# Performance work log

Hardware: AMD Instinct MI355X
Metric: run time of the kernel (lower is better)

## Reference

```python
import jax, jax.numpy as jnp
import numpy as np

DIM = 768
NUM_HEADS = 12
HEAD_DIM = DIM // NUM_HEADS
SCALE = HEAD_DIM ** -0.5
B, N = 16, 640  # N = 8*8 + 24*24


def setup_inputs() -> dict:
    key = jax.random.key(0)
    ks = jax.random.split(key, 4)
    x = jax.random.normal(ks[0], (B, N, DIM), dtype=jnp.float32)
    # weights stored input-major: y = x @ W + b (equiv. to torch Linear with W = weight.T)
    qkv_w = jax.random.normal(ks[1], (DIM, 3 * DIM), dtype=jnp.float32) * (DIM ** -0.5)
    qkv_b = jnp.zeros((3 * DIM,), dtype=jnp.float32)
    proj_w = jax.random.normal(ks[2], (DIM, DIM), dtype=jnp.float32) * (DIM ** -0.5)
    proj_b = jnp.zeros((DIM,), dtype=jnp.float32)
    w = jnp.ones((2,), dtype=jnp.float32)
    return {"x": x, "qkv_w": qkv_w, "qkv_b": qkv_b, "proj_w": proj_w,
            "proj_b": proj_b, "w": w, "t_h": 8, "t_w": 8, "s_h": 24, "s_w": 24}


def reference(x, qkv_w, qkv_b, proj_w, proj_b, w, t_h, t_w, s_h, s_w):
    b, n, c = x.shape
    qkv = (x @ qkv_w + qkv_b).reshape(b, n, 3, NUM_HEADS, HEAD_DIM)
    qkv = jnp.transpose(qkv, (2, 0, 3, 1, 4))  # [3, B, H, N, D]
    q, k, v = qkv[0], qkv[1], qkv[2]
    attn = jnp.einsum('bhnd,bhmd->bhnm', q, k) * SCALE  # [B,H,N,N]
    attn0 = jax.nn.softmax(attn, axis=-1)
    attn1 = jnp.square(jax.nn.relu(attn))
    ws = jax.nn.softmax(w)  # exp(w_i)/sum(exp(w)) blend weights
    attn = attn0 * ws[0] + attn1 * ws[1]
    out = jnp.einsum('bhnm,bhmd->bhnd', attn, v)  # [B,H,N,D]
    out = jnp.transpose(out, (0, 2, 1, 3)).reshape(b, n, c)
    return out @ proj_w + proj_b
```

## Files before the change

### kernel.cpp

```cpp
#include <hip/hip_runtime.h>
#include <hip/hip_bf16.h>

typedef __attribute__((ext_vector_type(8))) short short8;
typedef __attribute__((ext_vector_type(4))) float floatx4;
typedef __hip_bfloat16 bf16;

#define DIM 768
#define NH 12
#define HD 64
#define BB 16
#define NN 640
#define BH (BB*NH)
#define MROWS (BB*NN)
#define QKVN (3*DIM)
#define QSCALE 0.18033688011113205f
#define LN2SQ 0.4804530139182014f

#define CVT_BLK (MROWS*DIM/4/256)
#define TRQ_BLK ((QKVN/32)*(DIM/32))
#define TRP_BLK ((DIM/32)*(DIM/32))

__device__ __forceinline__ floatx4 mfma16(short8 a, short8 b, floatx4 c) {
    return __builtin_amdgcn_mfma_f32_16x16x32_bf16(a, b, c, 0, 0, 0);
}

__device__ __forceinline__ void async_ld16(const bf16* g, bf16* l) {
    __builtin_amdgcn_global_load_lds(
        (const __attribute__((address_space(1))) void*)g,
        (__attribute__((address_space(3))) void*)l, 16, 0, 0);
}

__device__ __forceinline__ unsigned pack_trunc(float a, float b) {
    return __builtin_amdgcn_perm(__float_as_uint(b), __float_as_uint(a), 0x07060302u);
}

__device__ __forceinline__ unsigned pack_rne(float a, float b) {
    unsigned sa = (unsigned)__bfloat16_as_ushort(__float2bfloat16(a));
    unsigned sb = (unsigned)__bfloat16_as_ushort(__float2bfloat16(b));
    return sa | (sb << 16);
}

__device__ __forceinline__ float fexp2(float x) {
#if __has_builtin(__builtin_amdgcn_exp2f)
    return __builtin_amdgcn_exp2f(x);
#else
    return exp2f(x);
#endif
}

__global__ void prep_all(const float* __restrict__ x,
                         const float* __restrict__ qkv_w,
                         const float* __restrict__ proj_w,
                         bf16* __restrict__ xb,
                         bf16* __restrict__ qwT,
                         bf16* __restrict__ pwT)
{
    __shared__ float tile[32][33];
    const int id = blockIdx.x;
    const int t = threadIdx.x;

    if (id < CVT_BLK) {
        int i = id * 256 + t;
        float4 v = ((const float4*)x)[i];
        *(uint2*)(xb + (size_t)i * 4) =
            make_uint2(pack_rne(v.x, v.y), pack_rne(v.z, v.w));
        return;
    }

    const float* src; bf16* dst; int C, bx, by;
    if (id < CVT_BLK + TRQ_BLK) {
        int j = id - CVT_BLK;
        bx = j % (QKVN/32); by = j / (QKVN/32);
        src = qkv_w; dst = qwT; C = QKVN;
    } else {
        int j = id - CVT_BLK - TRQ_BLK;
        bx = j % (DIM/32); by = j / (DIM/32);
        src = proj_w; dst = pwT; C = DIM;
    }
    const int R = DIM;
    const int tx = t & 31, ty = t >> 5;
    for (int j = 0; j < 4; ++j)
        tile[ty + j*8][tx] = src[(size_t)(by*32 + ty + j*8) * C + bx*32 + tx];
    __syncthreads();
    for (int j = 0; j < 4; ++j)
        dst[(size_t)(bx*32 + ty + j*8) * R + by*32 + tx] = __float2bfloat16(tile[tx][ty + j*8]);
}

template<int MODE>
__global__ __launch_bounds__(256) void gemm_bt(
    const bf16* __restrict__ A, const bf16* __restrict__ B, const float* __restrict__ bias,
    int M, int N, int K,
    bf16* __restrict__ outb, bf16* __restrict__ vTo, float* __restrict__ outf)
{
    __shared__ __align__(16) bf16 As[2][128*64];
    __shared__ __align__(16) bf16 Bs[2][128*64];

    const int t = threadIdx.x;
    const int lane = t & 63, wave = t >> 6;
    const int l15 = lane & 15, quad = lane >> 4;
    const int wm = (wave >> 1) * 64, wn = (wave & 1) * 64;

    constexpr int GX  = (MODE == 0) ? (QKVN/128) : (DIM/128);
    constexpr int NWG = GX * (MROWS/128);
    constexpr int CHUNK = NWG / 8;
    int lin = blockIdx.y * GX + blockIdx.x;
    lin = (lin & 7) * CHUNK + (lin >> 3);
    const int m0 = (lin / GX) * 128, n0 = (lin % GX) * 128;

    floatx4 acc[4][4];
    floatx4 zero = {0.f, 0.f, 0.f, 0.f};
    for (int i = 0; i < 4; ++i)
        for (int j = 0; j < 4; ++j)
            acc[i][j] = zero;

    const int trow = t >> 3;
    const int gc = ((t & 7) ^ (trow & 7)) << 3;
    const bf16* aA = A + (size_t)(m0 + trow) * K + gc;
    const bf16* aB = B + (size_t)(n0 + trow) * K + gc;
    const int lb = wave * 512;

    for (int s = 0; s < 4; ++s) {
        async_ld16(aA + (size_t)s*32*K, &As[0][s*2048 + lb]);
        async_ld16(aB + (size_t)s*32*K, &Bs[0][s*2048 + lb]);
    }

    const int sw = l15 & 7;
    const int nit = K >> 6;
    for (int kt = 0; kt < nit; ++kt) {
        const int cur = kt & 1;
        __syncthreads();
        if (kt + 1 < nit) {
            const bf16* pA = aA + (size_t)(kt+1)*64;
            const bf16* pB = aB + (size_t)(kt+1)*64;
            for (int s = 0; s < 4; ++s) {
                async_ld16(pA + (size_t)s*32*K, &As[cur^1][s*2048 + lb]);
                async_ld16(pB + (size_t)s*32*K, &Bs[cur^1][s*2048 + lb]);
            }
        }
        short8 af0[4], af1[4], bf0[4], bf1[4];
        for (int fm = 0; fm < 4; ++fm) {
            int base = (wm + fm*16 + l15) * 64 + ((quad ^ sw) << 3);
            af0[fm] = *(const short8*)(&As[cur][base]);
            af1[fm] = *(const short8*)(&As[cur][base ^ 32]);
        }
        for (int fn = 0; fn < 4; ++fn) {
            int base = (wn + fn*16 + l15) * 64 + ((quad ^ sw) << 3);
            bf0[fn] = *(const short8*)(&Bs[cur][base]);
            bf1[fn] = *(const short8*)(&Bs[cur][base ^ 32]);
        }
        for (int fm = 0; fm < 4; ++fm)
            for (int fn = 0; fn < 4; ++fn) {
                acc[fm][fn] = mfma16(bf0[fn], af0[fm], acc[fm][fn]);
                acc[fm][fn] = mfma16(bf1[fn], af1[fm], acc[fm][fn]);
            }
    }

    if (MODE == 0 && n0 >= 2*DIM) {
        bf16* S = &As[0][0] + wave * 2048;
        unsigned short* Su = (unsigned short*)S;
        const int bh   = (m0 / NN) * NH + ((n0 + wn) >> 6) - 24;
        const int tokb = (m0 % NN) + wm;
        const int dl = lane >> 2, cc = (lane & 3) * 16;
        for (int fn = 0; fn < 4; ++fn) {
            int nb = n0 + wn + fn*16 + quad*4;
            float4 bv = *(const float4*)(bias + nb);
            float bvr[4] = {bv.x, bv.y, bv.z, bv.w};
            for (int fm = 0; fm < 4; ++fm) {
#pragma unroll
                for (int r = 0; r < 4; ++r) {
                    float v = acc[fm][fn][r] + bvr[r];
                    Su[(quad*4 + r)*72 + fm*16 + l15] =
                        (unsigned short)(__float_as_uint(v) >> 16);
                }
            }
            uint4 r0 = *(const uint4*)(S + dl*72 + cc);
            uint4 r1 = *(const uint4*)(S + dl*72 + cc + 8);
            bf16* dst = vTo + ((size_t)bh * HD + fn*16 + dl) * NN + tokb + cc;
            *(uint4*)dst = r0;
            *(uint4*)(dst + 8) = r1;
        }
        return;
    }

    for (int fm = 0; fm < 4; ++fm) {
        int m = m0 + wm + fm*16 + l15;
        if (MODE == 0) {
            bf16* row = outb + (size_t)m * N;
            for (int fn = 0; fn < 4; ++fn) {
                int n = n0 + wn + fn*16 + quad*4;
                float4 bv = *(const float4*)(bias + n);
                float v0 = acc[fm][fn][0] + bv.x;
                float v1 = acc[fm][fn][1] + bv.y;
                float v2 = acc[fm][fn][2] + bv.z;
                float v3 = acc[fm][fn][3] + bv.w;
                if (n < DIM) {
                    v0 *= QSCALE; v1 *= QSCALE; v2 *= QSCALE; v3 *= QSCALE;
                }
                *(uint2*)(row + n) = make_uint2(pack_rne(v0, v1), pack_rne(v2, v3));
            }
        } else {
            float* row = outf + (size_t)m * N;
            for (int fn = 0; fn < 4; ++fn) {
                int n = n0 + wn + fn*16 + quad*4;
                float4 bv = *(const float4*)(bias + n);
                float4 v;
                v.x = acc[fm][fn][0] + bv.x;
                v.y = acc[fm][fn][1] + bv.y;
                v.z = acc[fm][fn][2] + bv.z;
                v.w = acc[fm][fn][3] + bv.w;
                *(float4*)(row + n) = v;
            }
        }
    }
}

__global__ __launch_bounds__(256) void attn_kernel(
    const bf16* __restrict__ qkv, const bf16* __restrict__ vT,
    const float* __restrict__ w2, bf16* __restrict__ ao)
{
    int lin = blockIdx.y * BH + blockIdx.x;
    int j = lin >> 3;
    const int bh = (lin & 7) + 8 * (j / 10);
    const int qt = j % 10;
    const int b = bh / NH, h = bh - b * NH;
    const int t = threadIdx.x;
    const int wave = t >> 6, lane = t & 63;
    const int l15 = lane & 15, quad = lane >> 4;
    const int qrow0 = qt * 64 + wave * 16;

    float w0 = w2[0], w1 = w2[1];
    float wmx = fmaxf(w0, w1);
    float e0 = __expf(w0 - wmx), e1 = __expf(w1 - wmx);
    float ws0 = e0 / (e0 + e1);
    float ws1 = (1.0f - ws0) * LN2SQ;

    __shared__ __align__(16) bf16 Kb[2][64*64];
    __shared__ __align__(16) bf16 Vb[2][64*64];
    __shared__ __align__(16) bf16 Ps[4][16*72];
    __shared__ __align__(16) bf16 Pr[4][16*72];

    const bf16* kb = qkv + (size_t)(b*NN)*QKVN + DIM + h*HD;
    const bf16* vb = vT + (size_t)bh * HD * NN;

    const bf16* qr = qkv + (size_t)(b*NN + qrow0 + l15) * QKVN + h*HD;
    short8 aq0 = *(const short8*)(qr + quad*8);
    short8 aq1 = *(const short8*)(qr + 32 + quad*8);

    const int srow = t >> 3;
    const int gc   = ((lane & 7) ^ (lane >> 3)) << 3;
    const bf16* kst = kb + (size_t)srow * QKVN + gc;
    const bf16* vst = vb + (size_t)srow * NN + gc;
    const int lb0 = (wave * 64) * 8;
    const int lb1 = (256 + wave * 64) * 8;

    async_ld16(kst,                     &Kb[0][lb0]);
    async_ld16(kst + (size_t)32 * QKVN, &Kb[0][lb1]);
    async_ld16(vst,                     &Vb[0][lb0]);
    async_ld16(vst + (size_t)32 * NN,   &Vb[0][lb1]);

    floatx4 zero = {0.f, 0.f, 0.f, 0.f};
    floatx4 accS[4], accR[4];
    for (int i = 0; i < 4; ++i) { accS[i] = zero; accR[i] = zero; }
    float lsum = 0.f;

    const int sw = l15 & 7;
    const int fbase = l15 * 64 + ((quad ^ sw) << 3);

    unsigned* PsW = (unsigned*)&Ps[wave][0];
    unsigned* PrW = (unsigned*)&Pr[wave][0];
    const int wb = l15*36 + quad*2;
    const bf16* PsR = &Ps[wave][l15*72 + quad*8];
    const bf16* PrR = &Pr[wave][l15*72 + quad*8];

#pragma unroll 2
    for (int kt = 0; kt < 10; ++kt) {
        const int cur = kt & 1;
        __syncthreads();
        if (kt + 1 < 10) {
            kst += (size_t)64 * QKVN;
            vst += 64;
            async_ld16(kst,                     &Kb[cur^1][lb0]);
            async_ld16(kst + (size_t)32 * QKVN, &Kb[cur^1][lb1]);
            async_ld16(vst,                     &Vb[cur^1][lb0]);
            async_ld16(vst + (size_t)32 * NN,   &Vb[cur^1][lb1]);
        }

        const bf16* Kc = &Kb[cur][0];
        const bf16* Vc = &Vb[cur][0];

        floatx4 s[4];
        for (int I = 0; I < 4; ++I) {
            short8 aklo = *(const short8*)(Kc + fbase + I*1024);
            short8 akhi = *(const short8*)(Kc + ((fbase + I*1024) ^ 32));
            s[I] = zero;
            s[I] = mfma16(aklo, aq0, s[I]);
            s[I] = mfma16(akhi, aq1, s[I]);
        }

        short8 bvlo[4], bvhi[4];
        for (int dt = 0; dt < 4; ++dt) {
            bvlo[dt] = *(const short8*)(Vc + fbase + dt*1024);
            bvhi[dt] = *(const short8*)(Vc + ((fbase + dt*1024) ^ 32));
        }

        for (int I = 0; I < 4; ++I) {
            float ex[4], rq[4];
            for (int r = 0; r < 4; ++r) {
                ex[r] = fexp2(s[I][r]);
                float m = fmaxf(s[I][r], 0.f);
                rq[r] = m * m;
                lsum += ex[r];
            }
            *(uint2*)(PsW + wb + I*8) = make_uint2(pack_trunc(ex[0],ex[1]), pack_trunc(ex[2],ex[3]));
            *(uint2*)(PrW + wb + I*8) = make_uint2(pack_trunc(rq[0],rq[1]), pack_trunc(rq[2],rq[3]));
        }

        short8 paSlo = *(const short8*)PsR;
        short8 paShi = *(const short8*)(PsR + 32);
        short8 paRlo = *(const short8*)PrR;
        short8 paRhi = *(const short8*)(PrR + 32);

        for (int dt = 0; dt < 4; ++dt) {
            accS[dt] = mfma16(paSlo, bvlo[dt], accS[dt]);
            accS[dt] = mfma16(paShi, bvhi[dt], accS[dt]);
            accR[dt] = mfma16(paRlo, bvlo[dt], accR[dt]);
            accR[dt] = mfma16(paRhi, bvhi[dt], accR[dt]);
        }
    }

    lsum += __shfl_xor(lsum, 16);
    lsum += __shfl_xor(lsum, 32);
    float invq[4];
    for (int r = 0; r < 4; ++r)
        invq[r] = 1.0f / __shfl(lsum, quad*4 + r);

    for (int dt = 0; dt < 4; ++dt) {
        for (int r = 0; r < 4; ++r) {
            float v = ws0 * accS[dt][r] * invq[r] + ws1 * accR[dt][r];
            int tok = qrow0 + quad*4 + r;
            ao[((size_t)(b * NN + tok)) * DIM + h * HD + dt*16 + l15] = __float2bfloat16(v);
        }
    }
}


extern "C" void kernel_launch(void* const* d_in, const int* in_sizes, int n_in,
                              void* d_out, int out_size, void* d_ws, size_t ws_size,
                              hipStream_t stream) {
    const float* x      = (const float*)d_in[0];
    const float* qkv_w  = (const float*)d_in[1];
    const float* qkv_b  = (const float*)d_in[2];
    const float* proj_w = (const float*)d_in[3];
    const float* proj_b = (const float*)d_in[4];
    const float* w2     = (const float*)d_in[5];
    float* out = (float*)d_out;

    bf16* xb   = (bf16*)d_ws;
    bf16* qwT  = xb   + (size_t)MROWS * DIM;
    bf16* pwT  = qwT  + (size_t)QKVN * DIM;
    bf16* qkvb = pwT  + (size_t)DIM * DIM;
    bf16* vT   = qkvb + (size_t)MROWS * QKVN;
    bf16* ao   = xb;

    prep_all<<<CVT_BLK + TRQ_BLK + TRP_BLK, 256, 0, stream>>>(
        x, qkv_w, proj_w, xb, qwT, pwT);

    gemm_bt<0><<<dim3(QKVN / 128, MROWS / 128), 256, 0, stream>>>(
        xb, qwT, qkv_b, MROWS, QKVN, DIM, qkvb, vT, nullptr);

    attn_kernel<<<dim3(BH, NN / 64), 256, 0, stream>>>(qkvb, vT, w2, ao);

    gemm_bt<1><<<dim3(DIM / 128, MROWS / 128), 256, 0, stream>>>(
        ao, pwT, proj_b, MROWS, DIM, DIM, nullptr, nullptr, out);
}
```

Before: 217.7 us.

## Use 128x192 tiles for QKV GEMM and 128-query attention blocks

Adds a dedicated QKV GEMM kernel with 128x192 output tiles (4x6 MFMA fragments per wave) and an XCD-aware block remap, splitting the V-transpose epilogue per 16-column fragment. The attention kernel now uses 512 threads covering 128 query rows per block, so each K/V tile loaded into LDS is shared by twice as many query rows, halving K/V global traffic. The larger accumulator arrays raise register pressure and the bigger attention blocks cut the block count, which may lower occupancy.

```diff
diff --git a/kernel.cpp b/kernel.cpp
--- a/kernel.cpp
+++ b/kernel.cpp
@@ -84,6 +84,139 @@
     __syncthreads();
     for (int j = 0; j < 4; ++j)
         dst[(size_t)(bx*32 + ty + j*8) * R + by*32 + tx] = __float2bfloat16(tile[tx][ty + j*8]);
+}
+
+__global__ __launch_bounds__(256) void gemm_qkv(
+    const bf16* __restrict__ A, const bf16* __restrict__ B, const float* __restrict__ bias,
+    bf16* __restrict__ outb, bf16* __restrict__ vTo)
+{
+    constexpr int K = DIM;
+    constexpr int N = QKVN;
+    constexpr int GX = N / 192;
+    constexpr int NWG = GX * (MROWS / 128);
+    constexpr int CHUNK = NWG / 8;
+
+    __shared__ __align__(16) bf16 As[2][128*64];
+    __shared__ __align__(16) bf16 Bs[2][192*64];
+
+    const int t = threadIdx.x;
+    const int lane = t & 63, wave = t >> 6;
+    const int l15 = lane & 15, quad = lane >> 4;
+    const int wm = (wave >> 1) * 64;
+    const int wn = (wave & 1) * 96;
+
+    int lin = blockIdx.x;
+    lin = (lin & 7) * CHUNK + (lin >> 3);
+    const int m0 = (lin / GX) * 128, n0 = (lin % GX) * 192;
+
+    floatx4 acc[4][6];
+    floatx4 zero = {0.f, 0.f, 0.f, 0.f};
+#pragma unroll
+    for (int i = 0; i < 4; ++i)
+#pragma unroll
+        for (int j = 0; j < 6; ++j)
+            acc[i][j] = zero;
+
+    const int trow = t >> 3;
+    const int gc = ((t & 7) ^ (trow & 7)) << 3;
+    const bf16* aA = A + (size_t)(m0 + trow) * K + gc;
+    const bf16* aB = B + (size_t)(n0 + trow) * K + gc;
+    const int lb = wave * 512;
+
+#pragma unroll
+    for (int s = 0; s < 4; ++s)
+        async_ld16(aA + (size_t)s*32*K, &As[0][s*2048 + lb]);
+#pragma unroll
+    for (int s = 0; s < 6; ++s)
+        async_ld16(aB + (size_t)s*32*K, &Bs[0][s*2048 + lb]);
+
+    const int sw = l15 & 7;
+    const int nit = K >> 6;
+    for (int kt = 0; kt < nit; ++kt) {
+        const int cur = kt & 1;
+        __syncthreads();
+        if (kt + 1 < nit) {
+            const bf16* pA = aA + (size_t)(kt+1)*64;
+            const bf16* pB = aB + (size_t)(kt+1)*64;
+#pragma unroll
+            for (int s = 0; s < 4; ++s)
+                async_ld16(pA + (size_t)s*32*K, &As[cur^1][s*2048 + lb]);
+#pragma unroll
+            for (int s = 0; s < 6; ++s)
+                async_ld16(pB + (size_t)s*32*K, &Bs[cur^1][s*2048 + lb]);
+        }
+        short8 af0[4], af1[4], bf0[6], bf1[6];
+#pragma unroll
+        for (int fm = 0; fm < 4; ++fm) {
+            int base = (wm + fm*16 + l15) * 64 + ((quad ^ sw) << 3);
+            af0[fm] = *(const short8*)(&As[cur][base]);
+            af1[fm] = *(const short8*)(&As[cur][base ^ 32]);
+        }
+#pragma unroll
+        for (int fn = 0; fn < 6; ++fn) {
+            int base = (wn + fn*16 + l15) * 64 + ((quad ^ sw) << 3);
+            bf0[fn] = *(const short8*)(&Bs[cur][base]);
+            bf1[fn] = *(const short8*)(&Bs[cur][base ^ 32]);
+        }
+#pragma unroll
+        for (int fm = 0; fm < 4; ++fm)
+#pragma unroll
+            for (int fn = 0; fn < 6; ++fn) {
+                acc[fm][fn] = mfma16(bf0[fn], af0[fm], acc[fm][fn]);
+                acc[fm][fn] = mfma16(bf1[fn], af1[fm], acc[fm][fn]);
+            }
+    }
+
+    const int mb = m0 + wm;
+    const int nb = n0 + wn;
+
+    if (n0 >= 2*DIM) {
+        bf16* S = &As[0][0] + wave * 2048;
+        unsigned short* Su = (unsigned short*)S;
+        const int batch = mb / NN;
+        const int tokb = mb % NN;
+        const int dl = lane >> 2, cc = (lane & 3) * 16;
+#pragma unroll
+        for (int fn = 0; fn < 6; ++fn) {
+            int cb = nb + fn*16;
+            int bh = batch * NH + ((cb - 2*DIM) >> 6);
+            int dbase = cb & 63;
+            float4 bv = *(const float4*)(bias + cb + quad*4);
+            float bvr[4] = {bv.x, bv.y, bv.z, bv.w};
+#pragma unroll
+            for (int fm = 0; fm < 4; ++fm) {
+#pragma unroll
+                for (int r = 0; r < 4; ++r) {
+                    float v = acc[fm][fn][r] + bvr[r];
+                    Su[(quad*4 + r)*72 + fm*16 + l15] =
+                        (unsigned short)(__float_as_uint(v) >> 16);
+                }
+            }
+            uint4 r0 = *(const uint4*)(S + dl*72 + cc);
+            uint4 r1 = *(const uint4*)(S + dl*72 + cc + 8);
+            bf16* dst = vTo + ((size_t)bh * HD + dbase + dl) * NN + tokb + cc;
+            *(uint4*)dst = r0;
+            *(uint4*)(dst + 8) = r1;
+        }
+        return;
+    }
+
+#pragma unroll
+    for (int fm = 0; fm < 4; ++fm) {
+        int m = mb + fm*16 + l15;
+        bf16* row = outb + (size_t)m * N;
+#pragma unroll
+        for (int fn = 0; fn < 6; ++fn) {
+            int n = nb + fn*16 + quad*4;
+            float4 bv = *(const float4*)(bias + n);
+            float v0 = acc[fm][fn][0] + bv.x;
+            float v1 = acc[fm][fn][1] + bv.y;
+            float v2 = acc[fm][fn][2] + bv.z;
+            float v3 = acc[fm][fn][3] + bv.w;
+            if (n < DIM) { v0 *= QSCALE; v1 *= QSCALE; v2 *= QSCALE; v3 *= QSCALE; }
+            *(uint2*)(row + n) = make_uint2(pack_rne(v0, v1), pack_rne(v2, v3));
+        }
+    }
 }
 
 template<int MODE>
@@ -155,78 +288,35 @@
             }
     }
 
-    if (MODE == 0 && n0 >= 2*DIM) {
-        bf16* S = &As[0][0] + wave * 2048;
-        unsigned short* Su = (unsigned short*)S;
-        const int bh   = (m0 / NN) * NH + ((n0 + wn) >> 6) - 24;
-        const int tokb = (m0 % NN) + wm;
-        const int dl = lane >> 2, cc = (lane & 3) * 16;
-        for (int fn = 0; fn < 4; ++fn) {
-            int nb = n0 + wn + fn*16 + quad*4;
-            float4 bv = *(const float4*)(bias + nb);
-            float bvr[4] = {bv.x, bv.y, bv.z, bv.w};
-            for (int fm = 0; fm < 4; ++fm) {
-#pragma unroll
-                for (int r = 0; r < 4; ++r) {
-                    float v = acc[fm][fn][r] + bvr[r];
-                    Su[(quad*4 + r)*72 + fm*16 + l15] =
-                        (unsigned short)(__float_as_uint(v) >> 16);
-                }
-            }
-            uint4 r0 = *(const uint4*)(S + dl*72 + cc);
-            uint4 r1 = *(const uint4*)(S + dl*72 + cc + 8);
-            bf16* dst = vTo + ((size_t)bh * HD + fn*16 + dl) * NN + tokb + cc;
-            *(uint4*)dst = r0;
-            *(uint4*)(dst + 8) = r1;
-        }
-        return;
-    }
-
     for (int fm = 0; fm < 4; ++fm) {
         int m = m0 + wm + fm*16 + l15;
-        if (MODE == 0) {
-            bf16* row = outb + (size_t)m * N;
-            for (int fn = 0; fn < 4; ++fn) {
-                int n = n0 + wn + fn*16 + quad*4;
-                float4 bv = *(const float4*)(bias + n);
-                float v0 = acc[fm][fn][0] + bv.x;
-                float v1 = acc[fm][fn][1] + bv.y;
-                float v2 = acc[fm][fn][2] + bv.z;
-                float v3 = acc[fm][fn][3] + bv.w;
-                if (n < DIM) {
-                    v0 *= QSCALE; v1 *= QSCALE; v2 *= QSCALE; v3 *= QSCALE;
-                }
-                *(uint2*)(row + n) = make_uint2(pack_rne(v0, v1), pack_rne(v2, v3));
-            }
-        } else {
-            float* row = outf + (size_t)m * N;
-            for (int fn = 0; fn < 4; ++fn) {
-                int n = n0 + wn + fn*16 + quad*4;
-                float4 bv = *(const float4*)(bias + n);
-                float4 v;
-                v.x = acc[fm][fn][0] + bv.x;
-                v.y = acc[fm][fn][1] + bv.y;
-                v.z = acc[fm][fn][2] + bv.z;
-                v.w = acc[fm][fn][3] + bv.w;
-                *(float4*)(row + n) = v;
-            }
-        }
-    }
-}
-
-__global__ __launch_bounds__(256) void attn_kernel(
+        float* row = outf + (size_t)m * N;
+        for (int fn = 0; fn < 4; ++fn) {
+            int n = n0 + wn + fn*16 + quad*4;
+            float4 bv = *(const float4*)(bias + n);
+            float4 v;
+            v.x = acc[fm][fn][0] + bv.x;
+            v.y = acc[fm][fn][1] + bv.y;
+            v.z = acc[fm][fn][2] + bv.z;
+            v.w = acc[fm][fn][3] + bv.w;
+            *(float4*)(row + n) = v;
+        }
+    }
+}
+
+__global__ __launch_bounds__(512) void attn_kernel(
     const bf16* __restrict__ qkv, const bf16* __restrict__ vT,
     const float* __restrict__ w2, bf16* __restrict__ ao)
 {
     int lin = blockIdx.y * BH + blockIdx.x;
     int j = lin >> 3;
-    const int bh = (lin & 7) + 8 * (j / 10);
-    const int qt = j % 10;
+    const int bh = (lin & 7) + 8 * (j / 5);
+    const int qt = j % 5;
     const int b = bh / NH, h = bh - b * NH;
     const int t = threadIdx.x;
     const int wave = t >> 6, lane = t & 63;
     const int l15 = lane & 15, quad = lane >> 4;
-    const int qrow0 = qt * 64 + wave * 16;
+    const int qrow0 = qt * 128 + wave * 16;
 
     float w0 = w2[0], w1 = w2[1];
     float wmx = fmaxf(w0, w1);
@@ -236,8 +326,8 @@
 
     __shared__ __align__(16) bf16 Kb[2][64*64];
     __shared__ __align__(16) bf16 Vb[2][64*64];
-    __shared__ __align__(16) bf16 Ps[4][16*72];
-    __shared__ __align__(16) bf16 Pr[4][16*72];
+    __shared__ __align__(16) bf16 Ps[8][16*72];
+    __shared__ __align__(16) bf16 Pr[8][16*72];
 
     const bf16* kb = qkv + (size_t)(b*NN)*QKVN + DIM + h*HD;
     const bf16* vb = vT + (size_t)bh * HD * NN;
@@ -247,16 +337,13 @@
     short8 aq1 = *(const short8*)(qr + 32 + quad*8);
 
     const int srow = t >> 3;
-    const int gc   = ((lane & 7) ^ (lane >> 3)) << 3;
+    const int gc   = ((t & 7) ^ (srow & 7)) << 3;
     const bf16* kst = kb + (size_t)srow * QKVN + gc;
     const bf16* vst = vb + (size_t)srow * NN + gc;
-    const int lb0 = (wave * 64) * 8;
-    const int lb1 = (256 + wave * 64) * 8;
-
-    async_ld16(kst,                     &Kb[0][lb0]);
-    async_ld16(kst + (size_t)32 * QKVN, &Kb[0][lb1]);
-    async_ld16(vst,                     &Vb[0][lb0]);
-    async_ld16(vst + (size_t)32 * NN,   &Vb[0][lb1]);
+    const int lb = t * 8;
+
+    async_ld16(kst, &Kb[0][lb]);
+    async_ld16(vst, &Vb[0][lb]);
 
     floatx4 zero = {0.f, 0.f, 0.f, 0.f};
     floatx4 accS[4], accR[4];
@@ -279,10 +366,8 @@
         if (kt + 1 < 10) {
             kst += (size_t)64 * QKVN;
             vst += 64;
-            async_ld16(kst,                     &Kb[cur^1][lb0]);
-            async_ld16(kst + (size_t)32 * QKVN, &Kb[cur^1][lb1]);
-            async_ld16(vst,                     &Vb[cur^1][lb0]);
-            async_ld16(vst + (size_t)32 * NN,   &Vb[cur^1][lb1]);
+            async_ld16(kst, &Kb[cur^1][lb]);
+            async_ld16(vst, &Vb[cur^1][lb]);
         }
 
         const bf16* Kc = &Kb[cur][0];
@@ -365,10 +450,10 @@
     prep_all<<<CVT_BLK + TRQ_BLK + TRP_BLK, 256, 0, stream>>>(
         x, qkv_w, proj_w, xb, qwT, pwT);
 
-    gemm_bt<0><<<dim3(QKVN / 128, MROWS / 128), 256, 0, stream>>>(
-        xb, qwT, qkv_b, MROWS, QKVN, DIM, qkvb, vT, nullptr);
-
-    attn_kernel<<<dim3(BH, NN / 64), 256, 0, stream>>>(qkvb, vT, w2, ao);
+    gemm_qkv<<<dim3((QKVN/192) * (MROWS/128)), 256, 0, stream>>>(
+        xb, qwT, qkv_b, qkvb, vT);
+
+    attn_kernel<<<dim3(BH, NN / 128), 512, 0, stream>>>(qkvb, vT, w2, ao);
 
     gemm_bt<1><<<dim3(DIM / 128, MROWS / 128), 256, 0, stream>>>(
         ao, pwT, proj_b, MROWS, DIM, DIM, nullptr, nullptr, out);
```

Result: slower. 245.2 us (+12.6%).
